# Kernel optimization log

Measured on AMD Instinct MI355X. Metric: run time of the kernel, lower is better.

## Reference

```python
import jax, jax.numpy as jnp
import numpy as np

LAM = 0.1   # smooth_param
EPS = 1e-8  # torch cosine_similarity eps


def setup_inputs() -> dict:
    key = jax.random.key(0)
    k1, k2, k3 = jax.random.split(key, 3)
    B, num_supp, num_query, T, D = 8, 5, 128, 16, 2048
    supp = jax.random.normal(k1, (B, num_supp, T, D), jnp.float32)
    query = jax.random.normal(k2, (B, num_query, T, D), jnp.float32)
    query_ys = jax.random.randint(k3, (B * num_query,), 0, num_supp)
    return {"supp": supp, "query": query, "query_ys": query_ys}


def _cosine_dist(supp, query):
    # supp: (B, ns, T, D), query: (B, nq, T, D)
    # dist[b,q,s,l,m] = 1 - cos(supp[b,s,l], query[b,q,m]); batch order (b,q,s)
    B, ns, T, D = supp.shape
    nq = query.shape[1]
    dots = jnp.einsum('bsld,bqmd->bqslm', supp, query)
    sn = jnp.linalg.norm(supp, axis=-1)   # (B, ns, T)
    qn = jnp.linalg.norm(query, axis=-1)  # (B, nq, T)
    denom = jnp.maximum(sn[:, None, :, :, None] * qn[:, :, None, None, :], EPS)
    dist = 1.0 - dots / denom
    return dist.reshape(B * nq * ns, T, T)


def _dtw(dist):
    # Relaxed (soft-min) OTAM band DP. dist: (N, T, T) -> (N,)
    # opt grid is (T, T+2) with zero-padded columns m=0 and m=T+1.
    N, T, _ = dist.shape
    dist_pad = jnp.pad(dist, ((0, 0), (0, 0), (1, 1)))  # (N, T, T+2)
    # Row l=0: opt[0,m] = cumsum of dist_pad[0, :m+1]
    row0 = jnp.cumsum(dist_pad[:, 0, :], axis=-1)  # (N, T+2)

    m_idx = jnp.arange(1, T + 2)
    boundary = (m_idx == 1) | (m_idx == T + 1)  # 3-way softmin only at band edges

    def row_step(prev_row, dist_row):
        # prev_row: (N, T+2) = opt[l-1]; dist_row: (N, T+2) = dist_pad[:, l]
        def col_step(left, xs):
            diag, up, d, is_b = xs  # each (N,) except is_b scalar bool
            s2 = jnp.logaddexp(-diag / LAM, -left / LAM)        # {diag, left}
            s3 = jnp.logaddexp(s2, -up / LAM)                   # + {up}
            val = -LAM * jnp.where(is_b, s3, s2) + d
            return val, val

        xs = (prev_row[:, :-1].T, prev_row[:, 1:].T, dist_row[:, 1:].T, boundary)
        init = jnp.zeros((N,), dist_row.dtype)  # opt[l, 0] = 0
        _, cols = jax.lax.scan(col_step, init, xs)  # (T+1, N)
        new_row = jnp.concatenate([init[:, None], cols.T], axis=1)  # (N, T+2)
        return new_row, None

    rows = jnp.swapaxes(dist_pad[:, 1:, :], 0, 1)  # (T-1, N, T+2)
    final_row, _ = jax.lax.scan(row_step, row0, rows)
    return final_row[:, -1]  # opt[:, T-1, T+1]


def _cross_entropy(logits, labels):
    logp = jax.nn.log_softmax(logits, axis=-1)
    return -jnp.mean(jnp.take_along_axis(logp, labels[:, None], axis=1))


def reference(supp, query, query_ys):
    ns = supp.shape[1]
    dist = _cosine_dist(supp, query)            # (B*nq*ns, T, T)
    tam1 = _dtw(dist).reshape(-1, ns)           # forward-direction alignment
    tam2 = _dtw(dist[:, ::-1, ::-1]).reshape(-1, ns)  # flipped (dims 1,2)
    loss1 = _cross_entropy(-tam1, query_ys)
    loss2 = _cross_entropy(-tam2, query_ys)
    loss = 0.5 * (loss1 + loss2)
    tam = 0.5 * (tam1 + tam2)
    return loss, tam
```

## Files before the change

kernel.cpp:

```cpp
#include <hip/hip_runtime.h>
#include <hip/hip_bf16.h>

#define NB   8
#define NS   5
#define NQ   128
#define TT   16
#define DD   2048
#define NROW 1024
#define NSROW (NB * NS * TT)
#define KSL  512
#define LAMI 10.0f
#define LAMF 0.1f

typedef __attribute__((ext_vector_type(8))) short  short8;
typedef __attribute__((ext_vector_type(4))) float  float4v;

static __device__ __forceinline__ unsigned int cvtpk(float x, float y) {
    unsigned int r;
    asm("v_cvt_pk_bf16_f32 %0, %1, %2" : "=v"(r) : "v"(x), "v"(y));
    return r;
}

static __device__ __forceinline__ float dpp_shr1(float x) {
    int r = __builtin_amdgcn_update_dpp(0, __builtin_bit_cast(int, x),
                                        0x138 , 0xF, 0xF, true);
    return __builtin_bit_cast(float, r);
}

__global__ __launch_bounds__(256) void
preproc_supp(const float* __restrict__ supp, unsigned short* __restrict__ suppBf,
             float* __restrict__ suppSq, float* __restrict__ loss0)
{
    if (blockIdx.x == 0 && threadIdx.x == 0) loss0[0] = 0.f;
    const int wave = threadIdx.x >> 6, lane = threadIdx.x & 63;
    const int row = blockIdx.x * 4 + wave;
    const float* src = supp + (size_t)row * DD;
    unsigned short* dst = suppBf + (size_t)row * DD;
    float ss = 0.f;
    #pragma unroll
    for (int i = 0; i < 8; ++i) {
        float4 v = *reinterpret_cast<const float4*>(src + i * 256 + lane * 4);
        uint2 pv = { cvtpk(v.x, v.y), cvtpk(v.z, v.w) };
        *reinterpret_cast<uint2*>(dst + i * 256 + lane * 4) = pv;
        ss += v.x * v.x + v.y * v.y + v.z * v.z + v.w * v.w;
    }
    #pragma unroll
    for (int off = 32; off >= 1; off >>= 1) ss += __shfl_xor(ss, off, 64);
    if (lane == 0) suppSq[row] = ss;
}

__global__ __launch_bounds__(256, 4) void
dist_dtw_wave(const unsigned short* __restrict__ suppBf, const float* __restrict__ suppSq,
              const float* __restrict__ query, const int* __restrict__ ys,
              float* __restrict__ out)
{
    __shared__ __align__(16) float red[4][NS][64][4];
    __shared__ float qsqp[4][16];
    __shared__ float qq[16];
    __shared__ float distS[NS][TT][TT];
    __shared__ float ssqS[80];
    __shared__ float tamv[12];

    const int tid  = threadIdx.x;
    const int blk  = blockIdx.x;
    const int wave = tid >> 6;
    const int lane = tid & 63;
    const int fr   = lane & 15;
    const int quad = lane >> 4;

    if (tid < 80) ssqS[tid] = suppSq[(blk >> 7) * (NS * TT) + tid];

    const float* qp = query + (size_t)(blk * TT + fr) * DD + wave * KSL + quad * 8;
    const unsigned short* aps[NS];
    #pragma unroll
    for (int s = 0; s < NS; ++s)
        aps[s] = suppBf + ((size_t)((blk >> 7) * NS + s) * TT + fr) * DD
               + wave * KSL + quad * 8;

    float4v acc[NS];
    #pragma unroll
    for (int s = 0; s < NS; ++s) acc[s] = (float4v){0.f, 0.f, 0.f, 0.f};
    float ss = 0.f;

    #pragma unroll 2
    for (int kk = 0; kk < 16; ++kk) {
        float4 q0 = *reinterpret_cast<const float4*>(qp + kk * 32);
        float4 q1 = *reinterpret_cast<const float4*>(qp + kk * 32 + 4);
        union { unsigned int u[4]; short8 v; } qu;
        qu.u[0] = cvtpk(q0.x, q0.y); qu.u[1] = cvtpk(q0.z, q0.w);
        qu.u[2] = cvtpk(q1.x, q1.y); qu.u[3] = cvtpk(q1.z, q1.w);
        ss += q0.x*q0.x + q0.y*q0.y + q0.z*q0.z + q0.w*q0.w
            + q1.x*q1.x + q1.y*q1.y + q1.z*q1.z + q1.w*q1.w;
        #pragma unroll
        for (int s = 0; s < NS; ++s) {
            short8 a = *reinterpret_cast<const short8*>(aps[s] + kk * 32);
            acc[s] = __builtin_amdgcn_mfma_f32_16x16x32_bf16(a, qu.v, acc[s], 0, 0, 0);
        }
    }

    ss += __shfl_xor(ss, 16, 64);
    ss += __shfl_xor(ss, 32, 64);
    if (lane < 16) qsqp[wave][lane] = ss;
    #pragma unroll
    for (int s = 0; s < NS; ++s)
        *reinterpret_cast<float4v*>(red[wave][s][lane]) = acc[s];
    __syncthreads();

    if (tid < 16) qq[tid] = qsqp[0][tid] + qsqp[1][tid] + qsqp[2][tid] + qsqp[3][tid];
    __syncthreads();

    for (int p = tid; p < NS * 64; p += 256) {
        int t = p >> 6, ln = p & 63;
        float4v s4 = *reinterpret_cast<const float4v*>(red[0][t][ln]);
        #pragma unroll
        for (int w = 1; w < 4; ++w) {
            float4v r = *reinterpret_cast<const float4v*>(red[w][t][ln]);
            s4[0] += r[0]; s4[1] += r[1]; s4[2] += r[2]; s4[3] += r[3];
        }
        int m = ln & 15, qd = ln >> 4;
        float qn = sqrtf(qq[m]);
        #pragma unroll
        for (int r = 0; r < 4; ++r) {
            int l = qd * 4 + r;
            float denom = fmaxf(sqrtf(ssqS[t * 16 + l]) * qn, 1e-8f);
            distS[t][l][m] = 1.0f - s4[r] / denom;
        }
    }
    __syncthreads();

    {
        const int grp  = lane / 21;
        const int g    = lane - grp * 21;
        const int slot = wave * 3 + grp;
        float val = 0.f, vprev = 0.f;
        if (grp < 3 && slot < 10 && g <= 17) {
            const int s    = slot >> 1;
            const int dir  = slot & 1;
            const bool isb = (g == 1) | (g == 17);
            #pragma unroll
            for (int t = 1; t <= 32; ++t) {
                float left = dpp_shr1(val);
                float diag = dpp_shr1(vprev);
                int l = t - g;
                if (g >= 1 && l >= 0 && l <= 15) {
                    float d = 0.f;
                    if (g <= 16) d = dir ? distS[s][15 - l][16 - g] : distS[s][l][g - 1];
                    float nv;
                    if (l == 0) {
                        nv = left + d;
                    } else {
                        float am = -LAMI * diag, bm = -LAMI * left;
                        float mx = fmaxf(am, bm);
                        float s3 = 0.f;
                        if (isb) {
                            float cm = -LAMI * val;
                            float m3 = fmaxf(mx, cm);
                            s3 = __expf(cm - m3);
                            mx = m3;
                        }
                        float ssum = __expf(am - mx) + __expf(bm - mx) + s3;
                        nv = fmaf(-LAMF, mx + __logf(ssum), d);
                    }
                    vprev = val; val = nv;
                }
            }
            if (g == 17) tamv[slot] = val;
        }
    }
    __syncthreads();

    if (tid < NS) out[1 + blk * NS + tid] = 0.5f * (tamv[2 * tid] + tamv[2 * tid + 1]);
    if (tid == 0) {
        float t1v[NS], t2v[NS];
        #pragma unroll
        for (int s = 0; s < NS; ++s) { t1v[s] = tamv[2 * s]; t2v[s] = tamv[2 * s + 1]; }
        const int y = ys[blk];
        float mx1 = -t1v[0], mx2 = -t2v[0];
        #pragma unroll
        for (int s = 1; s < NS; ++s) { mx1 = fmaxf(mx1, -t1v[s]); mx2 = fmaxf(mx2, -t2v[s]); }
        float s1 = 0.f, s2 = 0.f;
        #pragma unroll
        for (int s = 0; s < NS; ++s) { s1 += __expf(-t1v[s] - mx1); s2 += __expf(-t2v[s] - mx2); }
        float lse1  = mx1 + __logf(s1);
        float lse2v = mx2 + __logf(s2);
        float ty1 = t1v[0], ty2 = t2v[0];
        #pragma unroll
        for (int s = 1; s < NS; ++s) { if (y == s) { ty1 = t1v[s]; ty2 = t2v[s]; } }
        float c = 0.5f * ((lse1 + ty1) + (lse2v + ty2));
        atomicAdd(out, c * (1.0f / (float)NROW));
    }
}

extern "C" void kernel_launch(void* const* d_in, const int* in_sizes, int n_in,
                              void* d_out, int out_size, void* d_ws, size_t ws_size,
                              hipStream_t stream) {
    const float* supp  = (const float*)d_in[0];
    const float* query = (const float*)d_in[1];
    const int*   ys    = (const int*)d_in[2];
    float* out = (float*)d_out;

    float* suppSq = (float*)d_ws;
    unsigned short* suppBf = (unsigned short*)(suppSq + NSROW);

    preproc_supp<<<NSROW / 4, 256, 0, stream>>>(supp, suppBf, suppSq, out);
    dist_dtw_wave<<<NROW, 256, 0, stream>>>(suppBf, suppSq, query, ys, out);
}
```

Measured before the change: 229.8 us.

## Pre-normalize and pack supp and query into MFMA-tiled bf16 layout

Adds a preprocessing kernel that L2-normalizes every supp and query row and writes them as bf16 in an MFMA-fragment-tiled layout. The main kernel then loads contiguous short8 fragments and skips the norm and division work. The old path is kept as a fallback when the workspace is too small. The cost is an extra full write and read of the query tensor in bf16.

```diff
diff --git a/kernel.cpp b/kernel.cpp
--- a/kernel.cpp
+++ b/kernel.cpp
@@ -3,12 +3,13 @@
 
 #define NB   8
 #define NS   5
-#define NQ   128
 #define TT   16
 #define DD   2048
 #define NROW 1024
-#define NSROW (NB * NS * TT)
-#define KSL  512
+#define NSROW 640
+#define NQROW 16384
+#define TOTROW 17024
+#define TILESH (TT * DD)
 #define LAMI 10.0f
 #define LAMF 0.1f
 
@@ -27,107 +28,11 @@
     return __builtin_bit_cast(float, r);
 }
 
-__global__ __launch_bounds__(256) void
-preproc_supp(const float* __restrict__ supp, unsigned short* __restrict__ suppBf,
-             float* __restrict__ suppSq, float* __restrict__ loss0)
-{
-    if (blockIdx.x == 0 && threadIdx.x == 0) loss0[0] = 0.f;
-    const int wave = threadIdx.x >> 6, lane = threadIdx.x & 63;
-    const int row = blockIdx.x * 4 + wave;
-    const float* src = supp + (size_t)row * DD;
-    unsigned short* dst = suppBf + (size_t)row * DD;
-    float ss = 0.f;
-    #pragma unroll
-    for (int i = 0; i < 8; ++i) {
-        float4 v = *reinterpret_cast<const float4*>(src + i * 256 + lane * 4);
-        uint2 pv = { cvtpk(v.x, v.y), cvtpk(v.z, v.w) };
-        *reinterpret_cast<uint2*>(dst + i * 256 + lane * 4) = pv;
-        ss += v.x * v.x + v.y * v.y + v.z * v.z + v.w * v.w;
-    }
-    #pragma unroll
-    for (int off = 32; off >= 1; off >>= 1) ss += __shfl_xor(ss, off, 64);
-    if (lane == 0) suppSq[row] = ss;
-}
-
-__global__ __launch_bounds__(256, 4) void
-dist_dtw_wave(const unsigned short* __restrict__ suppBf, const float* __restrict__ suppSq,
-              const float* __restrict__ query, const int* __restrict__ ys,
-              float* __restrict__ out)
-{
-    __shared__ __align__(16) float red[4][NS][64][4];
-    __shared__ float qsqp[4][16];
-    __shared__ float qq[16];
-    __shared__ float distS[NS][TT][TT];
-    __shared__ float ssqS[80];
-    __shared__ float tamv[12];
-
-    const int tid  = threadIdx.x;
-    const int blk  = blockIdx.x;
-    const int wave = tid >> 6;
-    const int lane = tid & 63;
-    const int fr   = lane & 15;
-    const int quad = lane >> 4;
-
-    if (tid < 80) ssqS[tid] = suppSq[(blk >> 7) * (NS * TT) + tid];
-
-    const float* qp = query + (size_t)(blk * TT + fr) * DD + wave * KSL + quad * 8;
-    const unsigned short* aps[NS];
-    #pragma unroll
-    for (int s = 0; s < NS; ++s)
-        aps[s] = suppBf + ((size_t)((blk >> 7) * NS + s) * TT + fr) * DD
-               + wave * KSL + quad * 8;
-
-    float4v acc[NS];
-    #pragma unroll
-    for (int s = 0; s < NS; ++s) acc[s] = (float4v){0.f, 0.f, 0.f, 0.f};
-    float ss = 0.f;
-
-    #pragma unroll 2
-    for (int kk = 0; kk < 16; ++kk) {
-        float4 q0 = *reinterpret_cast<const float4*>(qp + kk * 32);
-        float4 q1 = *reinterpret_cast<const float4*>(qp + kk * 32 + 4);
-        union { unsigned int u[4]; short8 v; } qu;
-        qu.u[0] = cvtpk(q0.x, q0.y); qu.u[1] = cvtpk(q0.z, q0.w);
-        qu.u[2] = cvtpk(q1.x, q1.y); qu.u[3] = cvtpk(q1.z, q1.w);
-        ss += q0.x*q0.x + q0.y*q0.y + q0.z*q0.z + q0.w*q0.w
-            + q1.x*q1.x + q1.y*q1.y + q1.z*q1.z + q1.w*q1.w;
-        #pragma unroll
-        for (int s = 0; s < NS; ++s) {
-            short8 a = *reinterpret_cast<const short8*>(aps[s] + kk * 32);
-            acc[s] = __builtin_amdgcn_mfma_f32_16x16x32_bf16(a, qu.v, acc[s], 0, 0, 0);
-        }
-    }
-
-    ss += __shfl_xor(ss, 16, 64);
-    ss += __shfl_xor(ss, 32, 64);
-    if (lane < 16) qsqp[wave][lane] = ss;
-    #pragma unroll
-    for (int s = 0; s < NS; ++s)
-        *reinterpret_cast<float4v*>(red[wave][s][lane]) = acc[s];
-    __syncthreads();
-
-    if (tid < 16) qq[tid] = qsqp[0][tid] + qsqp[1][tid] + qsqp[2][tid] + qsqp[3][tid];
-    __syncthreads();
-
-    for (int p = tid; p < NS * 64; p += 256) {
-        int t = p >> 6, ln = p & 63;
-        float4v s4 = *reinterpret_cast<const float4v*>(red[0][t][ln]);
-        #pragma unroll
-        for (int w = 1; w < 4; ++w) {
-            float4v r = *reinterpret_cast<const float4v*>(red[w][t][ln]);
-            s4[0] += r[0]; s4[1] += r[1]; s4[2] += r[2]; s4[3] += r[3];
-        }
-        int m = ln & 15, qd = ln >> 4;
-        float qn = sqrtf(qq[m]);
-        #pragma unroll
-        for (int r = 0; r < 4; ++r) {
-            int l = qd * 4 + r;
-            float denom = fmaxf(sqrtf(ssqS[t * 16 + l]) * qn, 1e-8f);
-            distS[t][l][m] = 1.0f - s4[r] / denom;
-        }
-    }
-    __syncthreads();
-
+static __device__ __forceinline__ void
+dtw_and_out(const float (*distS)[TT][TT], float* tamv, int tid, int blk,
+            const int* __restrict__ ys, float* __restrict__ out)
+{
+    const int wave = tid >> 6, lane = tid & 63;
     {
         const int grp  = lane / 21;
         const int g    = lane - grp * 21;
@@ -191,6 +96,214 @@
     }
 }
 
+__global__ __launch_bounds__(256) void
+preproc_pack(const float* __restrict__ supp, const float* __restrict__ query,
+             unsigned short* __restrict__ sPk, unsigned short* __restrict__ qPk,
+             float* __restrict__ loss0)
+{
+    if (blockIdx.x == 0 && threadIdx.x == 0) loss0[0] = 0.f;
+    const int wave = threadIdx.x >> 6, lane = threadIdx.x & 63;
+    const int row = blockIdx.x * 4 + wave;
+
+    const float* src;
+    unsigned short* dstTile;
+    int fr;
+    if (row < NSROW) {
+        src = supp + (size_t)row * DD;
+        dstTile = sPk + (size_t)(row >> 4) * TILESH;
+        fr = row & 15;
+    } else {
+        const int qr = row - NSROW;
+        src = query + (size_t)qr * DD;
+        dstTile = qPk + (size_t)(qr >> 4) * TILESH;
+        fr = qr & 15;
+    }
+
+    float4 v[4][2];
+    float ss = 0.f;
+    #pragma unroll
+    for (int it = 0; it < 4; ++it) {
+        v[it][0] = *reinterpret_cast<const float4*>(src + it * 512 + lane * 8);
+        v[it][1] = *reinterpret_cast<const float4*>(src + it * 512 + lane * 8 + 4);
+        #pragma unroll
+        for (int h = 0; h < 2; ++h)
+            ss += v[it][h].x * v[it][h].x + v[it][h].y * v[it][h].y
+                + v[it][h].z * v[it][h].z + v[it][h].w * v[it][h].w;
+    }
+    #pragma unroll
+    for (int off = 32; off >= 1; off >>= 1) ss += __shfl_xor(ss, off, 64);
+    const float rs = 1.0f / sqrtf(fmaxf(ss, 1e-16f));
+
+    #pragma unroll
+    for (int it = 0; it < 4; ++it) {
+        uint4 pv;
+        pv.x = cvtpk(v[it][0].x * rs, v[it][0].y * rs);
+        pv.y = cvtpk(v[it][0].z * rs, v[it][0].w * rs);
+        pv.z = cvtpk(v[it][1].x * rs, v[it][1].y * rs);
+        pv.w = cvtpk(v[it][1].z * rs, v[it][1].w * rs);
+        const int kk = it * 16 + (lane >> 2);
+        const int c  = lane & 3;
+        *reinterpret_cast<uint4*>(dstTile + kk * 512 + (c * 16 + fr) * 8) = pv;
+    }
+}
+
+__global__ __launch_bounds__(256, 4) void
+dist_dtw_pk(const unsigned short* __restrict__ sPk, const unsigned short* __restrict__ qPk,
+            const int* __restrict__ ys, float* __restrict__ out)
+{
+    __shared__ __align__(16) float red[4][NS][64][4];
+    __shared__ float distS[NS][TT][TT];
+    __shared__ float tamv[12];
+
+    const int tid  = threadIdx.x;
+    const int blk  = blockIdx.x;
+    const int wave = tid >> 6;
+    const int lane = tid & 63;
+
+    const unsigned short* qp = qPk + (size_t)blk * TILESH + (wave * 16) * 512 + lane * 8;
+    const unsigned short* sp = sPk + (size_t)(blk >> 7) * NS * TILESH
+                             + (wave * 16) * 512 + lane * 8;
+
+    float4v acc[NS];
+    #pragma unroll
+    for (int s = 0; s < NS; ++s) acc[s] = (float4v){0.f, 0.f, 0.f, 0.f};
+
+    #pragma unroll 2
+    for (int kk = 0; kk < 16; ++kk) {
+        short8 q = *reinterpret_cast<const short8*>(qp + kk * 512);
+        #pragma unroll
+        for (int s = 0; s < NS; ++s) {
+            short8 a = *reinterpret_cast<const short8*>(sp + (size_t)s * TILESH + kk * 512);
+            acc[s] = __builtin_amdgcn_mfma_f32_16x16x32_bf16(a, q, acc[s], 0, 0, 0);
+        }
+    }
+
+    #pragma unroll
+    for (int s = 0; s < NS; ++s)
+        *reinterpret_cast<float4v*>(red[wave][s][lane]) = acc[s];
+    __syncthreads();
+
+    for (int p = tid; p < NS * 64; p += 256) {
+        int t = p >> 6, ln = p & 63;
+        float4v s4 = *reinterpret_cast<const float4v*>(red[0][t][ln]);
+        #pragma unroll
+        for (int w = 1; w < 4; ++w) {
+            float4v r = *reinterpret_cast<const float4v*>(red[w][t][ln]);
+            s4[0] += r[0]; s4[1] += r[1]; s4[2] += r[2]; s4[3] += r[3];
+        }
+        int m = ln & 15, qd = ln >> 4;
+        #pragma unroll
+        for (int r = 0; r < 4; ++r) distS[t][qd * 4 + r][m] = 1.0f - s4[r];
+    }
+    __syncthreads();
+
+    dtw_and_out(distS, tamv, tid, blk, ys, out);
+}
+
+__global__ __launch_bounds__(256) void
+preproc_supp5(const float* __restrict__ supp, unsigned short* __restrict__ suppBf,
+              float* __restrict__ suppSq, float* __restrict__ loss0)
+{
+    if (blockIdx.x == 0 && threadIdx.x == 0) loss0[0] = 0.f;
+    const int wave = threadIdx.x >> 6, lane = threadIdx.x & 63;
+    const int row = blockIdx.x * 4 + wave;
+    const float* src = supp + (size_t)row * DD;
+    unsigned short* dst = suppBf + (size_t)row * DD;
+    float ss = 0.f;
+    #pragma unroll
+    for (int i = 0; i < 8; ++i) {
+        float4 v = *reinterpret_cast<const float4*>(src + i * 256 + lane * 4);
+        uint2 pv = { cvtpk(v.x, v.y), cvtpk(v.z, v.w) };
+        *reinterpret_cast<uint2*>(dst + i * 256 + lane * 4) = pv;
+        ss += v.x * v.x + v.y * v.y + v.z * v.z + v.w * v.w;
+    }
+    #pragma unroll
+    for (int off = 32; off >= 1; off >>= 1) ss += __shfl_xor(ss, off, 64);
+    if (lane == 0) suppSq[row] = ss;
+}
+
+__global__ __launch_bounds__(256, 4) void
+dist_dtw_wave5(const unsigned short* __restrict__ suppBf, const float* __restrict__ suppSq,
+               const float* __restrict__ query, const int* __restrict__ ys,
+               float* __restrict__ out)
+{
+    __shared__ __align__(16) float red[4][NS][64][4];
+    __shared__ float qsqp[4][16];
+    __shared__ float qq[16];
+    __shared__ float distS[NS][TT][TT];
+    __shared__ float ssqS[80];
+    __shared__ float tamv[12];
+
+    const int tid  = threadIdx.x;
+    const int blk  = blockIdx.x;
+    const int wave = tid >> 6;
+    const int lane = tid & 63;
+    const int fr   = lane & 15;
+    const int quad = lane >> 4;
+
+    if (tid < 80) ssqS[tid] = suppSq[(blk >> 7) * (NS * TT) + tid];
+
+    const float* qp = query + (size_t)(blk * TT + fr) * DD + wave * 512 + quad * 8;
+    const unsigned short* aps[NS];
+    #pragma unroll
+    for (int s = 0; s < NS; ++s)
+        aps[s] = suppBf + ((size_t)((blk >> 7) * NS + s) * TT + fr) * DD
+               + wave * 512 + quad * 8;
+
+    float4v acc[NS];
+    #pragma unroll
+    for (int s = 0; s < NS; ++s) acc[s] = (float4v){0.f, 0.f, 0.f, 0.f};
+    float ss = 0.f;
+
+    #pragma unroll 2
+    for (int kk = 0; kk < 16; ++kk) {
+        float4 q0 = *reinterpret_cast<const float4*>(qp + kk * 32);
+        float4 q1 = *reinterpret_cast<const float4*>(qp + kk * 32 + 4);
+        union { unsigned int u[4]; short8 v; } qu;
+        qu.u[0] = cvtpk(q0.x, q0.y); qu.u[1] = cvtpk(q0.z, q0.w);
+        qu.u[2] = cvtpk(q1.x, q1.y); qu.u[3] = cvtpk(q1.z, q1.w);
+        ss += q0.x*q0.x + q0.y*q0.y + q0.z*q0.z + q0.w*q0.w
+            + q1.x*q1.x + q1.y*q1.y + q1.z*q1.z + q1.w*q1.w;
+        #pragma unroll
+        for (int s = 0; s < NS; ++s) {
+            short8 a = *reinterpret_cast<const short8*>(aps[s] + kk * 32);
+            acc[s] = __builtin_amdgcn_mfma_f32_16x16x32_bf16(a, qu.v, acc[s], 0, 0, 0);
+        }
+    }
+
+    ss += __shfl_xor(ss, 16, 64);
+    ss += __shfl_xor(ss, 32, 64);
+    if (lane < 16) qsqp[wave][lane] = ss;
+    #pragma unroll
+    for (int s = 0; s < NS; ++s)
+        *reinterpret_cast<float4v*>(red[wave][s][lane]) = acc[s];
+    __syncthreads();
+
+    if (tid < 16) qq[tid] = qsqp[0][tid] + qsqp[1][tid] + qsqp[2][tid] + qsqp[3][tid];
+    __syncthreads();
+
+    for (int p = tid; p < NS * 64; p += 256) {
+        int t = p >> 6, ln = p & 63;
+        float4v s4 = *reinterpret_cast<const float4v*>(red[0][t][ln]);
+        #pragma unroll
+        for (int w = 1; w < 4; ++w) {
+            float4v r = *reinterpret_cast<const float4v*>(red[w][t][ln]);
+            s4[0] += r[0]; s4[1] += r[1]; s4[2] += r[2]; s4[3] += r[3];
+        }
+        int m = ln & 15, qd = ln >> 4;
+        float qn = sqrtf(qq[m]);
+        #pragma unroll
+        for (int r = 0; r < 4; ++r) {
+            int l = qd * 4 + r;
+            float denom = fmaxf(sqrtf(ssqS[t * 16 + l]) * qn, 1e-8f);
+            distS[t][l][m] = 1.0f - s4[r] / denom;
+        }
+    }
+    __syncthreads();
+
+    dtw_and_out(distS, tamv, tid, blk, ys, out);
+}
+
 extern "C" void kernel_launch(void* const* d_in, const int* in_sizes, int n_in,
                               void* d_out, int out_size, void* d_ws, size_t ws_size,
                               hipStream_t stream) {
@@ -199,9 +312,16 @@
     const int*   ys    = (const int*)d_in[2];
     float* out = (float*)d_out;
 
-    float* suppSq = (float*)d_ws;
-    unsigned short* suppBf = (unsigned short*)(suppSq + NSROW);
-
-    preproc_supp<<<NSROW / 4, 256, 0, stream>>>(supp, suppBf, suppSq, out);
-    dist_dtw_wave<<<NROW, 256, 0, stream>>>(suppBf, suppSq, query, ys, out);
-}
+    const size_t needA = (size_t)(NS * NB + NROW) * TILESH * 2;
+    if (ws_size >= needA) {
+        unsigned short* sPk = (unsigned short*)d_ws;
+        unsigned short* qPk = sPk + (size_t)NS * NB * TILESH;
+        preproc_pack<<<TOTROW / 4, 256, 0, stream>>>(supp, query, sPk, qPk, out);
+        dist_dtw_pk<<<NROW, 256, 0, stream>>>(sPk, qPk, ys, out);
+    } else {
+        float* suppSq = (float*)d_ws;
+        unsigned short* suppBf = (unsigned short*)(suppSq + NSROW);
+        preproc_supp5<<<NSROW / 4, 256, 0, stream>>>(supp, suppBf, suppSq, out);
+        dist_dtw_wave5<<<NROW, 256, 0, stream>>>(suppBf, suppSq, query, ys, out);
+    }
+}
```

New measurement: 264.8 us. 15.2% more time.

## Pre-normalize rows, pack support in MFMA fragment layout, stage query via LDS

Applied to the files above, without the earlier changes.

Support rows are normalized by their L2 norm before bf16 conversion and written in a tile layout that matches the MFMA A-fragment, so each lane reads one contiguous 16-byte chunk per k-step. Query rows are also normalized and converted once into a padded LDS tile that feeds the MFMA B operand, which removes the separate norm reductions and the division in the distance step. The intent is more coalesced support loads and less per-block arithmetic. In exchange the kernel uses about 64KB of LDS, occupancy drops to 2 blocks, and all query loads must finish before a barrier, which adds latency. Normalizing before bf16 rounding also changes numerics slightly, and the EPS clamp now applies to each norm separately rather than to their product.

```diff
diff --git a/kernel.cpp b/kernel.cpp
--- a/kernel.cpp
+++ b/kernel.cpp
@@ -3,12 +3,12 @@
 
 #define NB   8
 #define NS   5
-#define NQ   128
 #define TT   16
 #define DD   2048
 #define NROW 1024
-#define NSROW (NB * NS * TT)
-#define KSL  512
+#define NSROW 640
+#define TILESH (TT * DD)
+#define LDS_ROW 2056
 #define LAMI 10.0f
 #define LAMF 0.1f
 
@@ -27,107 +27,11 @@
     return __builtin_bit_cast(float, r);
 }
 
-__global__ __launch_bounds__(256) void
-preproc_supp(const float* __restrict__ supp, unsigned short* __restrict__ suppBf,
-             float* __restrict__ suppSq, float* __restrict__ loss0)
+static __device__ __forceinline__ void
+dtw_and_out(const float (*distS)[TT][TT], float* tamv, int tid, int blk,
+            const int* __restrict__ ys, float* __restrict__ out)
 {
-    if (blockIdx.x == 0 && threadIdx.x == 0) loss0[0] = 0.f;
-    const int wave = threadIdx.x >> 6, lane = threadIdx.x & 63;
-    const int row = blockIdx.x * 4 + wave;
-    const float* src = supp + (size_t)row * DD;
-    unsigned short* dst = suppBf + (size_t)row * DD;
-    float ss = 0.f;
-    #pragma unroll
-    for (int i = 0; i < 8; ++i) {
-        float4 v = *reinterpret_cast<const float4*>(src + i * 256 + lane * 4);
-        uint2 pv = { cvtpk(v.x, v.y), cvtpk(v.z, v.w) };
-        *reinterpret_cast<uint2*>(dst + i * 256 + lane * 4) = pv;
-        ss += v.x * v.x + v.y * v.y + v.z * v.z + v.w * v.w;
-    }
-    #pragma unroll
-    for (int off = 32; off >= 1; off >>= 1) ss += __shfl_xor(ss, off, 64);
-    if (lane == 0) suppSq[row] = ss;
-}
-
-__global__ __launch_bounds__(256, 4) void
-dist_dtw_wave(const unsigned short* __restrict__ suppBf, const float* __restrict__ suppSq,
-              const float* __restrict__ query, const int* __restrict__ ys,
-              float* __restrict__ out)
-{
-    __shared__ __align__(16) float red[4][NS][64][4];
-    __shared__ float qsqp[4][16];
-    __shared__ float qq[16];
-    __shared__ float distS[NS][TT][TT];
-    __shared__ float ssqS[80];
-    __shared__ float tamv[12];
-
-    const int tid  = threadIdx.x;
-    const int blk  = blockIdx.x;
-    const int wave = tid >> 6;
-    const int lane = tid & 63;
-    const int fr   = lane & 15;
-    const int quad = lane >> 4;
-
-    if (tid < 80) ssqS[tid] = suppSq[(blk >> 7) * (NS * TT) + tid];
-
-    const float* qp = query + (size_t)(blk * TT + fr) * DD + wave * KSL + quad * 8;
-    const unsigned short* aps[NS];
-    #pragma unroll
-    for (int s = 0; s < NS; ++s)
-        aps[s] = suppBf + ((size_t)((blk >> 7) * NS + s) * TT + fr) * DD
-               + wave * KSL + quad * 8;
-
-    float4v acc[NS];
-    #pragma unroll
-    for (int s = 0; s < NS; ++s) acc[s] = (float4v){0.f, 0.f, 0.f, 0.f};
-    float ss = 0.f;
-
-    #pragma unroll 2
-    for (int kk = 0; kk < 16; ++kk) {
-        float4 q0 = *reinterpret_cast<const float4*>(qp + kk * 32);
-        float4 q1 = *reinterpret_cast<const float4*>(qp + kk * 32 + 4);
-        union { unsigned int u[4]; short8 v; } qu;
-        qu.u[0] = cvtpk(q0.x, q0.y); qu.u[1] = cvtpk(q0.z, q0.w);
-        qu.u[2] = cvtpk(q1.x, q1.y); qu.u[3] = cvtpk(q1.z, q1.w);
-        ss += q0.x*q0.x + q0.y*q0.y + q0.z*q0.z + q0.w*q0.w
-            + q1.x*q1.x + q1.y*q1.y + q1.z*q1.z + q1.w*q1.w;
-        #pragma unroll
-        for (int s = 0; s < NS; ++s) {
-            short8 a = *reinterpret_cast<const short8*>(aps[s] + kk * 32);
-            acc[s] = __builtin_amdgcn_mfma_f32_16x16x32_bf16(a, qu.v, acc[s], 0, 0, 0);
-        }
-    }
-
-    ss += __shfl_xor(ss, 16, 64);
-    ss += __shfl_xor(ss, 32, 64);
-    if (lane < 16) qsqp[wave][lane] = ss;
-    #pragma unroll
-    for (int s = 0; s < NS; ++s)
-        *reinterpret_cast<float4v*>(red[wave][s][lane]) = acc[s];
-    __syncthreads();
-
-    if (tid < 16) qq[tid] = qsqp[0][tid] + qsqp[1][tid] + qsqp[2][tid] + qsqp[3][tid];
-    __syncthreads();
-
-    for (int p = tid; p < NS * 64; p += 256) {
-        int t = p >> 6, ln = p & 63;
-        float4v s4 = *reinterpret_cast<const float4v*>(red[0][t][ln]);
-        #pragma unroll
-        for (int w = 1; w < 4; ++w) {
-            float4v r = *reinterpret_cast<const float4v*>(red[w][t][ln]);
-            s4[0] += r[0]; s4[1] += r[1]; s4[2] += r[2]; s4[3] += r[3];
-        }
-        int m = ln & 15, qd = ln >> 4;
-        float qn = sqrtf(qq[m]);
-        #pragma unroll
-        for (int r = 0; r < 4; ++r) {
-            int l = qd * 4 + r;
-            float denom = fmaxf(sqrtf(ssqS[t * 16 + l]) * qn, 1e-8f);
-            distS[t][l][m] = 1.0f - s4[r] / denom;
-        }
-    }
-    __syncthreads();
-
+    const int wave = tid >> 6, lane = tid & 63;
     {
         const int grp  = lane / 21;
         const int g    = lane - grp * 21;
@@ -191,6 +95,125 @@
     }
 }
 
+__global__ __launch_bounds__(256) void
+pack_supp(const float* __restrict__ supp, unsigned short* __restrict__ sPk,
+          float* __restrict__ loss0)
+{
+    if (blockIdx.x == 0 && threadIdx.x == 0) loss0[0] = 0.f;
+    const int wave = threadIdx.x >> 6, lane = threadIdx.x & 63;
+    const int row = blockIdx.x * 4 + wave;
+    const float* src = supp + (size_t)row * DD;
+    unsigned short* dstTile = sPk + (size_t)(row >> 4) * TILESH;
+    const int fr = row & 15;
+
+    float4 v[4][2];
+    float ss = 0.f;
+    #pragma unroll
+    for (int it = 0; it < 4; ++it) {
+        v[it][0] = *reinterpret_cast<const float4*>(src + it * 512 + lane * 8);
+        v[it][1] = *reinterpret_cast<const float4*>(src + it * 512 + lane * 8 + 4);
+        #pragma unroll
+        for (int h = 0; h < 2; ++h)
+            ss += v[it][h].x * v[it][h].x + v[it][h].y * v[it][h].y
+                + v[it][h].z * v[it][h].z + v[it][h].w * v[it][h].w;
+    }
+    #pragma unroll
+    for (int off = 32; off >= 1; off >>= 1) ss += __shfl_xor(ss, off, 64);
+    const float rs = 1.0f / sqrtf(fmaxf(ss, 1e-16f));
+
+    #pragma unroll
+    for (int it = 0; it < 4; ++it) {
+        uint4 pv;
+        pv.x = cvtpk(v[it][0].x * rs, v[it][0].y * rs);
+        pv.y = cvtpk(v[it][0].z * rs, v[it][0].w * rs);
+        pv.z = cvtpk(v[it][1].x * rs, v[it][1].y * rs);
+        pv.w = cvtpk(v[it][1].z * rs, v[it][1].w * rs);
+        const int kk = it * 16 + (lane >> 2);
+        const int c  = lane & 3;
+        *reinterpret_cast<uint4*>(dstTile + kk * 512 + (c * 16 + fr) * 8) = pv;
+    }
+}
+
+__global__ __launch_bounds__(256, 2) void
+dist_dtw_fused(const unsigned short* __restrict__ sPk, const float* __restrict__ query,
+               const int* __restrict__ ys, float* __restrict__ out)
+{
+    __shared__ __align__(16) unsigned char smem[TT * LDS_ROW * 2];
+    unsigned short (*sB)[LDS_ROW] = reinterpret_cast<unsigned short(*)[LDS_ROW]>(smem);
+    float (*red)[NS][64][4] = reinterpret_cast<float(*)[NS][64][4]>(smem);
+    float (*distS)[TT][TT]  = reinterpret_cast<float(*)[TT][TT]>(smem + 20480);
+    float* tamv             = reinterpret_cast<float*>(smem + 25600);
+
+    const int tid  = threadIdx.x;
+    const int blk  = blockIdx.x;
+    const int wave = tid >> 6;
+    const int lane = tid & 63;
+    const int fr   = lane & 15;
+    const int quad = lane >> 4;
+
+    #pragma unroll
+    for (int j = 0; j < 4; ++j) {
+        const int r = wave * 4 + j;
+        const float* src = query + (size_t)(blk * TT + r) * DD;
+        float4 v[8];
+        float ss = 0.f;
+        #pragma unroll
+        for (int i = 0; i < 8; ++i) {
+            v[i] = *reinterpret_cast<const float4*>(src + i * 256 + lane * 4);
+            ss += v[i].x * v[i].x + v[i].y * v[i].y + v[i].z * v[i].z + v[i].w * v[i].w;
+        }
+        #pragma unroll
+        for (int off = 32; off >= 1; off >>= 1) ss += __shfl_xor(ss, off, 64);
+        const float rs = 1.0f / sqrtf(fmaxf(ss, 1e-16f));
+        #pragma unroll
+        for (int i = 0; i < 8; ++i) {
+            uint2 pv = { cvtpk(v[i].x * rs, v[i].y * rs), cvtpk(v[i].z * rs, v[i].w * rs) };
+            *reinterpret_cast<uint2*>(&sB[r][i * 256 + lane * 4]) = pv;
+        }
+    }
+    __syncthreads();
+
+    float4v acc[NS];
+    #pragma unroll
+    for (int s = 0; s < NS; ++s) acc[s] = (float4v){0.f, 0.f, 0.f, 0.f};
+
+    const unsigned short* sp = sPk + (size_t)(blk >> 7) * NS * TILESH
+                             + (size_t)(wave * 16) * 512 + lane * 8;
+    const unsigned short* bb = &sB[fr][(wave * 16) * 32 + quad * 8];
+
+    #pragma unroll 2
+    for (int kk = 0; kk < 16; ++kk) {
+        short8 b = *reinterpret_cast<const short8*>(bb + kk * 32);
+        #pragma unroll
+        for (int s = 0; s < NS; ++s) {
+            short8 a = *reinterpret_cast<const short8*>(sp + (size_t)s * TILESH + kk * 512);
+            acc[s] = __builtin_amdgcn_mfma_f32_16x16x32_bf16(a, b, acc[s], 0, 0, 0);
+        }
+    }
+    __syncthreads();
+
+    #pragma unroll
+    for (int s = 0; s < NS; ++s)
+        *reinterpret_cast<float4v*>(red[wave][s][lane]) = acc[s];
+    __syncthreads();
+
+    for (int p = tid; p < NS * 64; p += 256) {
+        int t = p >> 6, ln = p & 63;
+        float4v s4 = *reinterpret_cast<const float4v*>(red[0][t][ln]);
+        #pragma unroll
+        for (int w = 1; w < 4; ++w) {
+            float4v r = *reinterpret_cast<const float4v*>(red[w][t][ln]);
+            s4[0] += r[0]; s4[1] += r[1]; s4[2] += r[2]; s4[3] += r[3];
+        }
+        int m = ln & 15, qd = ln >> 4;
+        #pragma unroll
+        for (int r = 0; r < 4; ++r) distS[t][qd * 4 + r][m] = 1.0f - s4[r];
+    }
+    __syncthreads();
+
+    dtw_and_out(distS, tamv, tid, blk, ys, out);
+}
+
 extern "C" void kernel_launch(void* const* d_in, const int* in_sizes, int n_in,
                               void* d_out, int out_size, void* d_ws, size_t ws_size,
                               hipStream_t stream) {
@@ -199,9 +222,8 @@
     const int*   ys    = (const int*)d_in[2];
     float* out = (float*)d_out;
 
-    float* suppSq = (float*)d_ws;
-    unsigned short* suppBf = (unsigned short*)(suppSq + NSROW);
-
-    preproc_supp<<<NSROW / 4, 256, 0, stream>>>(supp, suppBf, suppSq, out);
-    dist_dtw_wave<<<NROW, 256, 0, stream>>>(suppBf, suppSq, query, ys, out);
-}
+    unsigned short* sPk = (unsigned short*)d_ws;
+
+    pack_supp<<<NSROW / 4, 256, 0, stream>>>(supp, sPk, out);
+    dist_dtw_fused<<<NROW, 256, 0, stream>>>(sPk, query, ys, out);
+}
```

Measured after the change: 225.3 us. 1.02x faster.
